# Optimization experiments

Measured on AMD Instinct MI355X. Metric: run time of the kernel, lower is better.

## Reference

```python
import jax, jax.numpy as jnp
import numpy as np

SIGMA = 0.3


def quat_mul(q, r):
    w1, x1, y1, z1 = q[..., 0], q[..., 1], q[..., 2], q[..., 3]
    w2, x2, y2, z2 = r[..., 0], r[..., 1], r[..., 2], r[..., 3]
    return jnp.stack([
        w1 * w2 - x1 * x2 - y1 * y2 - z1 * z2,
        w1 * x2 + x1 * w2 + y1 * z2 - z1 * y2,
        w1 * y2 - x1 * z2 + y1 * w2 + z1 * x2,
        w1 * z2 + x1 * y2 - y1 * x2 + z1 * w2,
    ], axis=-1)


def quat_conjugate(q):
    return q * jnp.array([1.0, -1.0, -1.0, -1.0], dtype=q.dtype)


def quat_rotate(q, v):
    v_quat = jnp.concatenate([jnp.zeros_like(v[..., :1]), v], axis=-1)
    return quat_mul(quat_mul(q, v_quat), quat_conjugate(q))[..., 1:]


def compute_adjacency_batch(x, sigma):
    pos = x[..., :3]
    diff = pos[:, :, None, :] - pos[:, None, :, :]
    dist_sq = jnp.sum(diff * diff, axis=-1)
    A = jnp.exp(-dist_sq / (sigma * sigma))
    I = jnp.eye(A.shape[-1], dtype=A.dtype)[None]
    A = A * (1.0 - I) + I
    return A / jnp.sum(A, axis=-1, keepdims=True)


def _mlp(x, params):
    # params: list of (W, b); GELU (exact erf, torch default) between layers
    n = len(params)
    for i, (W, b) in enumerate(params):
        x = x @ W + b
        if i < n - 1:
            x = jax.nn.gelu(x, approximate=False)
    return x


def _linear_params(key, din, dout, scale=0.05):
    k1, k2 = jax.random.split(key)
    W = jax.random.normal(k1, (din, dout), dtype=jnp.float32) * scale
    b = jax.random.normal(k2, (dout,), dtype=jnp.float32) * scale
    return W, b


def setup_inputs() -> dict:
    key = jax.random.key(0)
    B, N_p, M, D_o, D_p, H = 4, 32768, 64, 13, 13, 256
    ks = jax.random.split(key, 16)
    t = jax.random.uniform(ks[0], (), dtype=jnp.float32)
    x_p = jax.random.normal(ks[1], (B, N_p, D_p), dtype=jnp.float32)
    x_o = jax.random.normal(ks[2], (B, M, D_o), dtype=jnp.float32)
    S = jax.nn.softmax(jax.random.normal(ks[3], (B, N_p, M), dtype=jnp.float32), axis=-1)
    # edge_net: (2*D_o+3+1+1) -> H -> H -> D_o
    ew0, eb0 = _linear_params(ks[4], 2 * D_o + 5, H)
    ew1, eb1 = _linear_params(ks[5], H, H)
    ew2, eb2 = _linear_params(ks[6], H, D_o)
    # f_vel: (2*D_o+1) -> H -> H -> H -> 3
    vw0, vb0 = _linear_params(ks[7], 2 * D_o + 1, H)
    vw1, vb1 = _linear_params(ks[8], H, H)
    vw2, vb2 = _linear_params(ks[9], H, H)
    vw3, vb3 = _linear_params(ks[10], H, 3)
    # f_omega: same sizes
    ow0, ob0 = _linear_params(ks[11], 2 * D_o + 1, H)
    ow1, ob1 = _linear_params(ks[12], H, H)
    ow2, ob2 = _linear_params(ks[13], H, H)
    ow3, ob3 = _linear_params(ks[14], H, 3)
    return dict(t=t, x_p=x_p, x_o=x_o, S=S,
                ew0=ew0, eb0=eb0, ew1=ew1, eb1=eb1, ew2=ew2, eb2=eb2,
                vw0=vw0, vb0=vb0, vw1=vw1, vb1=vb1, vw2=vw2, vb2=vb2, vw3=vw3, vb3=vb3,
                ow0=ow0, ob0=ob0, ow1=ow1, ob1=ob1, ow2=ow2, ob2=ob2, ow3=ow3, ob3=ob3)


def reference(t, x_p, x_o, S,
              ew0, eb0, ew1, eb1, ew2, eb2,
              vw0, vb0, vw1, vb1, vw2, vb2, vw3, vb3,
              ow0, ob0, ow1, ob1, ow2, ob2, ow3, ob3):
    B, N_p, D_p = x_p.shape
    _, N_o, D_o = x_o.shape
    tt = jnp.reshape(jnp.asarray(t, x_o.dtype), ())

    # ---- object-object messaging ----
    A_obj = compute_adjacency_batch(x_o, sigma=SIGMA)          # [B,No,No]
    pos = x_o[..., :3]
    diff = pos[:, None, :, :] - pos[:, :, None, :]             # diff[b,i,j] = pos_j - pos_i
    distance = jnp.linalg.norm(diff, axis=-1, keepdims=True)
    h_i = jnp.broadcast_to(x_o[:, :, None, :], (B, N_o, N_o, D_o))
    h_j = jnp.broadcast_to(x_o[:, None, :, :], (B, N_o, N_o, D_o))
    t_edge = jnp.broadcast_to(tt, (B, N_o, N_o, 1))
    edge_input = jnp.concatenate([h_i, h_j, diff, distance, t_edge], axis=-1)
    edge_message = _mlp(edge_input, [(ew0, eb0), (ew1, eb1), (ew2, eb2)])  # [B,No,No,Do]
    m_obj = jnp.sum(A_obj[..., None] * edge_message, axis=2)   # [B,No,Do]

    COM_obj = x_o[:, :, :3]
    vel_obj = x_o[:, :, 3:6]
    quat_obj = x_o[:, :, 6:10]
    omega_obj = x_o[:, :, 10:13]

    t0 = jnp.broadcast_to(tt, (B, N_o, 1))
    node_in = jnp.concatenate([x_o, m_obj, t0], axis=-1)
    dx_o_vel = _mlp(node_in, [(vw0, vb0), (vw1, vb1), (vw2, vb2), (vw3, vb3)])
    dx_o_omega = _mlp(node_in, [(ow0, ob0), (ow1, ob1), (ow2, ob2), (ow3, ob3)])
    omega_quat = jnp.concatenate([jnp.zeros_like(omega_obj[..., :1]), omega_obj], axis=-1)
    dx_o_quat = 0.5 * quat_mul(omega_quat, quat_obj)
    dx_o = jnp.concatenate([vel_obj, dx_o_vel, dx_o_quat, dx_o_omega], axis=-1)

    # ---- particle rigid-transform branch ----
    pos_t0 = x_p[..., 10:13]
    local = pos_t0[:, :, None, :] - COM_obj[:, None, :, :]     # [B,Np,M,3]
    rot_local = quat_rotate(quat_obj[:, None, :, :], local)    # broadcast quats over particles
    pred_vel = vel_obj[:, None, :, :] + jnp.cross(
        jnp.broadcast_to(omega_obj[:, None, :, :], rot_local.shape), rot_local)
    final_vel = jnp.sum(S[..., None] * pred_vel, axis=2)       # [B,Np,3]

    current_vel = x_p[..., 3:6]
    dpos = final_vel
    dvel = final_vel - current_vel
    dquat = jnp.zeros_like(x_p[..., 6:10])
    dpos_t0 = jnp.zeros_like(x_p[..., 10:13])
    dx_p = jnp.concatenate([dpos, dvel, dquat, dpos_t0], axis=-1)
    return dx_p, dx_o
```

## Files before the change

kernel.cpp:

```cpp
#include <hip/hip_runtime.h>
#include <math.h>

typedef unsigned short u16;
typedef unsigned int   u32;

typedef __attribute__((ext_vector_type(8))) short short8;
typedef __attribute__((ext_vector_type(4))) float f32x4;

static constexpr int CB  = 4;
static constexpr int CNP = 32768;
static constexpr int CM  = 64;
static constexpr int CDO = 13;
static constexpr int CH  = 256;
static constexpr int DXP_ELEMS = CB * CNP * CDO;

static constexpr int WSB_W0 = 16384;
static constexpr int WSB_W1 = 32768;

__device__ __forceinline__ float bf2f(u16 v) { return __uint_as_float(((u32)v) << 16); }
__device__ __forceinline__ u16 f2bf(float f) {
    u32 u = __float_as_uint(f);
    u += 0x7fffu + ((u >> 16) & 1u);
    return (u16)(u >> 16);
}
__device__ __forceinline__ float gelu_f(float x) {
    float y = 0.7978845608028654f * (x + 0.044715f * x * x * x);
    float e = __expf(2.0f * y);
    float t = 1.0f - 2.0f / (e + 1.0f);
    return 0.5f * x * (1.0f + t);
}

__global__ __launch_bounds__(256) void k0_prep(const float* __restrict__ ew0,
                                               const float* __restrict__ ew1,
                                               u16* __restrict__ w0frag,
                                               u16* __restrict__ w1frag) {
    int idx = blockIdx.x * 256 + threadIdx.x;
    if (idx < 8192) {
        int j = idx & 7, lane = (idx >> 3) & 63, nt = idx >> 9;
        int k = (lane >> 4) * 8 + j, n = nt * 16 + (lane & 15);
        float v = (k < 31) ? ew0[k * CH + n] : 0.0f;
        w0frag[idx] = f2bf(v);
    } else if (idx < 73728) {
        int rel = idx - 8192;
        int j = rel & 7, lane = (rel >> 3) & 63, ktnt = rel >> 9;
        int nt = ktnt & 15, kt = ktnt >> 4;
        int k = kt * 32 + (lane >> 4) * 8 + j, n = nt * 16 + (lane & 15);
        w1frag[rel] = f2bf(ew1[k * CH + n]);
    }
}

__global__ __launch_bounds__(256) void k1_edge(const float* __restrict__ xo,
                                               const float* __restrict__ tp,
                                               const float* __restrict__ eb0,
                                               const float* __restrict__ eb1,
                                               const float* __restrict__ ew2,
                                               const float* __restrict__ eb2,
                                               const u16* __restrict__ w0frag,
                                               const u16* __restrict__ w1frag,
                                               float* __restrict__ mobj) {
    __shared__ float sXo[832];
    __shared__ float sAnorm[64];
    __shared__ float sInv;
    __shared__ float sBias[512];
    __shared__ float sW2[3456];
    __shared__ float sMsg[512];
    __shared__ __align__(16) u16 sIn[32 * 40];
    __shared__ __align__(16) u16 sH1[32 * 264];
    __shared__ __align__(16) u16 sH2T[256 * 36];

    const int tid  = threadIdx.x;
    const int blk  = blockIdx.x;
    const int b    = blk >> 6;
    const int i    = blk & 63;
    const int wave = tid >> 6;
    const int lane = tid & 63;
    const int quad = lane >> 4;
    const int mr   = lane & 15;
    const int mtile = wave & 1;
    const int nhalf = wave >> 1;

    for (int idx = tid; idx < 832; idx += 256) sXo[idx] = xo[(size_t)b * 832 + idx];
    sBias[tid]       = eb0[tid];
    sBias[256 + tid] = eb1[tid];
    for (int idx = tid; idx < 3456; idx += 256) sW2[idx] = (idx < 3328) ? ew2[idx] : 0.0f;
    __syncthreads();

    const float pix = sXo[i * 13 + 0], piy = sXo[i * 13 + 1], piz = sXo[i * 13 + 2];
    if (tid < 64) {
        float dx = pix - sXo[tid * 13 + 0];
        float dy = piy - sXo[tid * 13 + 1];
        float dz = piz - sXo[tid * 13 + 2];
        sAnorm[tid] = expf(-(dx * dx + dy * dy + dz * dz) * 11.111111111111111f);
    }
    __syncthreads();
    if (tid == 0) {
        float s = 0.0f;
        #pragma unroll
        for (int q = 0; q < 64; ++q) s += sAnorm[q];
        sInv = 1.0f / s;
    }
    __syncthreads();
    if (tid < 64) sAnorm[tid] *= sInv;
    const float tval = tp[0];

    float msum = (tid < 13) ? eb2[tid] : 0.0f;

    for (int pass = 0; pass < 2; ++pass) {
        const int j0 = pass * 32;
        for (int idx = tid; idx < 1024; idx += 256) {
            int e = idx >> 5, k = idx & 31;
            int j = j0 + e;
            float v;
            if (k < 13) v = sXo[i * 13 + k];
            else if (k < 26) v = sXo[j * 13 + (k - 13)];
            else if (k < 29) { int c = k - 26; v = sXo[j * 13 + c] - sXo[i * 13 + c]; }
            else if (k == 29) {
                float dx = sXo[j * 13 + 0] - pix;
                float dy = sXo[j * 13 + 1] - piy;
                float dz = sXo[j * 13 + 2] - piz;
                v = sqrtf(dx * dx + dy * dy + dz * dz);
            } else if (k == 30) v = tval;
            else v = 0.0f;
            sIn[e * 40 + k] = f2bf(v);
        }
        __syncthreads();

        {
            short8 afrag = *(const short8*)(sIn + (mtile * 16 + mr) * 40 + quad * 8);
            for (int p = 0; p < 4; ++p) {
                int nt = nhalf * 8 + p * 2;
                float bv0 = sBias[nt * 16 + mr];
                float bv1 = sBias[nt * 16 + 16 + mr];
                f32x4 acc0 = { bv0, bv0, bv0, bv0 };
                f32x4 acc1 = { bv1, bv1, bv1, bv1 };
                short8 bf0 = *(const short8*)(w0frag + (nt * 64 + lane) * 8);
                short8 bf1 = *(const short8*)(w0frag + ((nt + 1) * 64 + lane) * 8);
                acc0 = __builtin_amdgcn_mfma_f32_16x16x32_bf16(afrag, bf0, acc0, 0, 0, 0);
                acc1 = __builtin_amdgcn_mfma_f32_16x16x32_bf16(afrag, bf1, acc1, 0, 0, 0);
                #pragma unroll
                for (int r = 0; r < 4; ++r) {
                    int row = mtile * 16 + quad * 4 + r;
                    sH1[row * 264 + nt * 16 + mr]        = f2bf(gelu_f(acc0[r]));
                    sH1[row * 264 + (nt + 1) * 16 + mr]  = f2bf(gelu_f(acc1[r]));
                }
            }
        }
        __syncthreads();

        for (int p = 0; p < 4; ++p) {
            int nt = nhalf * 8 + p * 2;
            float bv0 = sBias[256 + nt * 16 + mr];
            float bv1 = sBias[256 + nt * 16 + 16 + mr];
            f32x4 acc0 = { bv0, bv0, bv0, bv0 };
            f32x4 acc1 = { bv1, bv1, bv1, bv1 };
            #pragma unroll
            for (int kt = 0; kt < 8; ++kt) {
                short8 a  = *(const short8*)(sH1 + (mtile * 16 + mr) * 264 + kt * 32 + quad * 8);
                short8 b0 = *(const short8*)(w1frag + ((kt * 16 + nt) * 64 + lane) * 8);
                short8 b1 = *(const short8*)(w1frag + ((kt * 16 + nt + 1) * 64 + lane) * 8);
                acc0 = __builtin_amdgcn_mfma_f32_16x16x32_bf16(a, b0, acc0, 0, 0, 0);
                acc1 = __builtin_amdgcn_mfma_f32_16x16x32_bf16(a, b1, acc1, 0, 0, 0);
            }
            u16 pk0[4], pk1[4];
            #pragma unroll
            for (int r = 0; r < 4; ++r) { pk0[r] = f2bf(gelu_f(acc0[r])); pk1[r] = f2bf(gelu_f(acc1[r])); }
            int n0 = nt * 16 + mr, n1 = (nt + 1) * 16 + mr;
            int eb = mtile * 16 + quad * 4;
            *(uint2*)(sH2T + n0 * 36 + eb) = *(const uint2*)pk0;
            *(uint2*)(sH2T + n1 * 36 + eb) = *(const uint2*)pk1;
        }
        __syncthreads();

        {
            const int e = tid & 31;
            const int g = tid >> 5;
            float acc0 = 0.0f, acc1 = 0.0f;
            #pragma unroll 8
            for (int n = 0; n < 256; ++n) {
                float h = bf2f(sH2T[n * 36 + e]);
                acc0 = fmaf(h, sW2[n * 13 + g], acc0);
                acc1 = fmaf(h, sW2[n * 13 + g + 8], acc1);
            }
            float aw = sAnorm[j0 + e];
            sMsg[e * 16 + g] = acc0 * aw;
            if (g < 5) sMsg[e * 16 + g + 8] = acc1 * aw;
        }
        __syncthreads();

        if (tid < 13) {
            float s = 0.0f;
            #pragma unroll
            for (int e = 0; e < 32; ++e) s += sMsg[e * 16 + tid];
            msum += s;
        }
        __syncthreads();
    }

    if (tid < 13) mobj[blk * 16 + tid] = msum;
}

__global__ __launch_bounds__(256) void k2_node(const float* __restrict__ xo,
                                               const float* __restrict__ tp,
                                               const float* __restrict__ mobj,
                                               const float* vw0, const float* vb0,
                                               const float* vw1, const float* vb1,
                                               const float* vw2, const float* vb2,
                                               const float* vw3, const float* vb3,
                                               const float* ow0, const float* ob0,
                                               const float* ow1, const float* ob1,
                                               const float* ow2, const float* ob2,
                                               const float* ow3, const float* ob3,
                                               float* __restrict__ out_dxo) {
    __shared__ float sIn[32];
    __shared__ float sA[256];
    __shared__ float sB[256];
    __shared__ float sPart[192];
    __shared__ float sOut[3];

    const int n   = blockIdx.x >> 1;
    const int ml  = blockIdx.x & 1;
    const int tid = threadIdx.x;

    const float* w0 = ml ? ow0 : vw0;  const float* b0 = ml ? ob0 : vb0;
    const float* w1 = ml ? ow1 : vw1;  const float* b1 = ml ? ob1 : vb1;
    const float* w2 = ml ? ow2 : vw2;  const float* b2 = ml ? ob2 : vb2;
    const float* w3 = ml ? ow3 : vw3;  const float* b3 = ml ? ob3 : vb3;

    const float* xrow = xo + (size_t)n * CDO;
    if (tid < 13)       sIn[tid] = xrow[tid];
    else if (tid < 26)  sIn[tid] = mobj[n * 16 + (tid - 13)];
    else if (tid == 26) sIn[26]  = tp[0];
    __syncthreads();

    float a = b0[tid];
    #pragma unroll
    for (int k = 0; k < 27; ++k) a = fmaf(sIn[k], w0[k * CH + tid], a);
    sA[tid] = gelu_f(a);
    __syncthreads();

    a = b1[tid];
    for (int k8 = 0; k8 < 32; ++k8) {
        float wv[8];
        #pragma unroll
        for (int u = 0; u < 8; ++u) wv[u] = w1[(k8 * 8 + u) * CH + tid];
        #pragma unroll
        for (int u = 0; u < 8; ++u) a = fmaf(sA[k8 * 8 + u], wv[u], a);
    }
    sB[tid] = gelu_f(a);
    __syncthreads();

    a = b2[tid];
    for (int k8 = 0; k8 < 32; ++k8) {
        float wv[8];
        #pragma unroll
        for (int u = 0; u < 8; ++u) wv[u] = w2[(k8 * 8 + u) * CH + tid];
        #pragma unroll
        for (int u = 0; u < 8; ++u) a = fmaf(sB[k8 * 8 + u], wv[u], a);
    }
    sA[tid] = gelu_f(a);
    __syncthreads();

    if (tid < 192) {
        int o = tid % 3, seg = tid / 3;
        float p = 0.0f;
        #pragma unroll
        for (int u = 0; u < 4; ++u) {
            int k = seg * 4 + u;
            p = fmaf(sA[k], w3[k * 3 + o], p);
        }
        sPart[tid] = p;
    }
    __syncthreads();
    if (tid < 3) {
        float s = b3[tid];
        for (int seg = 0; seg < 64; ++seg) s += sPart[seg * 3 + tid];
        sOut[tid] = s;
    }
    __syncthreads();

    if (tid == 0) {
        float* o = out_dxo + (size_t)n * CDO;
        if (ml == 0) {
            o[0] = xrow[3]; o[1] = xrow[4]; o[2] = xrow[5];
            o[3] = sOut[0]; o[4] = sOut[1]; o[5] = sOut[2];
        } else {
            float qw = xrow[6], qx = xrow[7], qy = xrow[8], qz = xrow[9];
            float ox = xrow[10], oy = xrow[11], oz = xrow[12];
            o[6] = -0.5f * (ox * qx + oy * qy + oz * qz);
            o[7] =  0.5f * (ox * qw + oy * qz - oz * qy);
            o[8] =  0.5f * (-ox * qz + oy * qw + oz * qx);
            o[9] =  0.5f * (ox * qy - oy * qx + oz * qw);
            o[10] = sOut[0]; o[11] = sOut[1]; o[12] = sOut[2];
        }
    }
}

__global__ __launch_bounds__(256) void k3_part(const float* __restrict__ xp,
                                               const float* __restrict__ S,
                                               const float* __restrict__ xo,
                                               float* __restrict__ out) {
    __shared__ float sXo[832];
    __shared__ float sPar[768];
    __shared__ __align__(16) float sXp[3328];
    __shared__ __align__(16) float sOutF[3328];

    const int tid  = threadIdx.x;
    const int blk  = blockIdx.x;
    const int pid0 = blk << 8;
    const int b    = pid0 >> 15;

    for (int idx = tid; idx < 832; idx += 256) sXo[idx] = xo[(size_t)b * 832 + idx];
    {
        const float4* src = (const float4*)(xp) + (size_t)blk * 832;
        float4* dst = (float4*)sXp;
        for (int idx = tid; idx < 832; idx += 256) dst[idx] = src[idx];
    }
    __syncthreads();

    if (tid < 64) {
        const int r = tid * CDO;
        float cx = sXo[r + 0], cy = sXo[r + 1], cz = sXo[r + 2];
        float vx = sXo[r + 3], vy = sXo[r + 4], vz = sXo[r + 5];
        float qw = sXo[r + 6], qx = sXo[r + 7], qy = sXo[r + 8], qz = sXo[r + 9];
        float ox = sXo[r + 10], oy = sXo[r + 11], oz = sXo[r + 12];
        float s2 = qw * qw - (qx * qx + qy * qy + qz * qz);
        float R00 = s2 + 2.f*qx*qx,        R01 = 2.f*qx*qy - 2.f*qw*qz, R02 = 2.f*qx*qz + 2.f*qw*qy;
        float R10 = 2.f*qy*qx + 2.f*qw*qz, R11 = s2 + 2.f*qy*qy,        R12 = 2.f*qy*qz - 2.f*qw*qx;
        float R20 = 2.f*qz*qx - 2.f*qw*qy, R21 = 2.f*qz*qy + 2.f*qw*qx, R22 = s2 + 2.f*qz*qz;
        float W00 = -oz*R10 + oy*R20, W01 = -oz*R11 + oy*R21, W02 = -oz*R12 + oy*R22;
        float W10 =  oz*R00 - ox*R20, W11 =  oz*R01 - ox*R21, W12 =  oz*R02 - ox*R22;
        float W20 = -oy*R00 + ox*R10, W21 = -oy*R01 + ox*R11, W22 = -oy*R02 + ox*R12;
        float* par = sPar + tid * 12;
        par[0] = vx - (W00*cx + W01*cy + W02*cz);
        par[1] = vy - (W10*cx + W11*cy + W12*cz);
        par[2] = vz - (W20*cx + W21*cy + W22*cz);
        par[3] = W00; par[4]  = W01; par[5]  = W02;
        par[6] = W10; par[7]  = W11; par[8]  = W12;
        par[9] = W20; par[10] = W21; par[11] = W22;
    }
    __syncthreads();

    const int p13 = tid * CDO;
    const float cvx = sXp[p13 + 3],  cvy = sXp[p13 + 4],  cvz = sXp[p13 + 5];
    const float px  = sXp[p13 + 10], py  = sXp[p13 + 11], pz  = sXp[p13 + 12];

    float fvx = 0.0f, fvy = 0.0f, fvz = 0.0f;
    const size_t pid = (size_t)pid0 + tid;
    const float4* srow = (const float4*)(S) + pid * 16;
    #pragma unroll
    for (int g = 0; g < 16; ++g) {
        float4 sv = srow[g];
        float sf[4] = { sv.x, sv.y, sv.z, sv.w };
        #pragma unroll
        for (int h = 0; h < 4; ++h) {
            float s = sf[h];
            const float* pp = sPar + (g * 4 + h) * 12;
            float tx = pp[0] + pp[3] * px + pp[4]  * py + pp[5]  * pz;
            float ty = pp[1] + pp[6] * px + pp[7]  * py + pp[8]  * pz;
            float tz = pp[2] + pp[9] * px + pp[10] * py + pp[11] * pz;
            fvx = fmaf(s, tx, fvx);
            fvy = fmaf(s, ty, fvy);
            fvz = fmaf(s, tz, fvz);
        }
    }

    sOutF[p13 + 0] = fvx;
    sOutF[p13 + 1] = fvy;
    sOutF[p13 + 2] = fvz;
    sOutF[p13 + 3] = fvx - cvx;
    sOutF[p13 + 4] = fvy - cvy;
    sOutF[p13 + 5] = fvz - cvz;
    #pragma unroll
    for (int q = 6; q < 13; ++q) sOutF[p13 + q] = 0.0f;
    __syncthreads();
    {
        float4* dstg = (float4*)(out) + (size_t)blk * 832;
        const float4* srcl = (const float4*)sOutF;
        for (int idx = tid; idx < 832; idx += 256) dstg[idx] = srcl[idx];
    }
}

extern "C" void kernel_launch(void* const* d_in, const int* in_sizes, int n_in,
                              void* d_out, int out_size, void* d_ws, size_t ws_size,
                              hipStream_t stream) {
    const float* t  = (const float*)d_in[0];
    const float* xp = (const float*)d_in[1];
    const float* xo = (const float*)d_in[2];
    const float* S  = (const float*)d_in[3];
    float* mobj  = (float*)d_ws;
    u16* w0frag  = (u16*)((char*)d_ws + WSB_W0);
    u16* w1frag  = (u16*)((char*)d_ws + WSB_W1);
    float* out = (float*)d_out;

    hipLaunchKernelGGL(k0_prep, dim3(288), dim3(256), 0, stream,
                       (const float*)d_in[4], (const float*)d_in[6], w0frag, w1frag);
    hipLaunchKernelGGL(k1_edge, dim3(256), dim3(256), 0, stream,
                       xo, t,
                       (const float*)d_in[5], (const float*)d_in[7],
                       (const float*)d_in[8], (const float*)d_in[9],
                       w0frag, w1frag, mobj);
    hipLaunchKernelGGL(k2_node, dim3(512), dim3(256), 0, stream,
                       xo, t, mobj,
                       (const float*)d_in[10], (const float*)d_in[11],
                       (const float*)d_in[12], (const float*)d_in[13],
                       (const float*)d_in[14], (const float*)d_in[15],
                       (const float*)d_in[16], (const float*)d_in[17],
                       (const float*)d_in[18], (const float*)d_in[19],
                       (const float*)d_in[20], (const float*)d_in[21],
                       (const float*)d_in[22], (const float*)d_in[23],
                       (const float*)d_in[24], (const float*)d_in[25],
                       out + DXP_ELEMS);
    hipLaunchKernelGGL(k3_part, dim3(512), dim3(256), 0, stream,
                       xp, S, xo, out);
}
```

Before: 205.9 us.

## Batch node MLPs onto bf16 MFMA and use MFMA for edge output layer

```diff
diff --git a/kernel.cpp b/kernel.cpp
--- a/kernel.cpp
+++ b/kernel.cpp
@@ -14,8 +14,19 @@
 static constexpr int CH  = 256;
 static constexpr int DXP_ELEMS = CB * CNP * CDO;
 
-static constexpr int WSB_W0 = 16384;
-static constexpr int WSB_W1 = 32768;
+static constexpr int WSB_FRAG = 16384;
+static constexpr int F_EW0 = 0;
+static constexpr int F_EW1 = 8192;
+static constexpr int F_EW2 = 73728;
+static constexpr int F_VW0 = 77824;
+static constexpr int F_VW1 = 86016;
+static constexpr int F_VW2 = 151552;
+static constexpr int F_VW3 = 217088;
+static constexpr int F_OW0 = 221184;
+static constexpr int F_OW1 = 229376;
+static constexpr int F_OW2 = 294912;
+static constexpr int F_OW3 = 360448;
+static constexpr int F_TOTAL = 364544;
 
 __device__ __forceinline__ float bf2f(u16 v) { return __uint_as_float(((u32)v) << 16); }
 __device__ __forceinline__ u16 f2bf(float f) {
@@ -30,43 +41,54 @@
     return 0.5f * x * (1.0f + t);
 }
 
-__global__ __launch_bounds__(256) void k0_prep(const float* __restrict__ ew0,
-                                               const float* __restrict__ ew1,
-                                               u16* __restrict__ w0frag,
-                                               u16* __restrict__ w1frag) {
+struct Segs { const float* src[11]; };
+
+__constant__
+static __device__ const int SEG_BASE[12] = {0, 8192, 73728, 77824, 86016, 151552,
+                                            217088, 221184, 229376, 294912, 360448, 364544};
+static __device__ const int SEG_K[11]  = {31, 256, 256, 27, 256, 256, 256, 27, 256, 256, 256};
+static __device__ const int SEG_N[11]  = {256, 256, 13, 256, 256, 256, 3, 256, 256, 256, 3};
+static __device__ const int SEG_NT[11] = {16, 16, 1, 16, 16, 16, 1, 16, 16, 16, 1};
+
+__global__ __launch_bounds__(256) void k0_prep(Segs segs, float* __restrict__ ws,
+                                               u16* __restrict__ wsFrag) {
     int idx = blockIdx.x * 256 + threadIdx.x;
-    if (idx < 8192) {
-        int j = idx & 7, lane = (idx >> 3) & 63, nt = idx >> 9;
-        int k = (lane >> 4) * 8 + j, n = nt * 16 + (lane & 15);
-        float v = (k < 31) ? ew0[k * CH + n] : 0.0f;
-        w0frag[idx] = f2bf(v);
-    } else if (idx < 73728) {
-        int rel = idx - 8192;
-        int j = rel & 7, lane = (rel >> 3) & 63, ktnt = rel >> 9;
-        int nt = ktnt & 15, kt = ktnt >> 4;
-        int k = kt * 32 + (lane >> 4) * 8 + j, n = nt * 16 + (lane & 15);
-        w1frag[rel] = f2bf(ew1[k * CH + n]);
-    }
+    if (idx < 4096) { ws[idx] = 0.0f; return; }
+    int f = idx - 4096;
+    if (f >= F_TOTAL) return;
+    int s = 0;
+    while (f >= SEG_BASE[s + 1]) ++s;
+    int rel = f - SEG_BASE[s];
+    int j = rel & 7, lane = (rel >> 3) & 63, t = rel >> 9;
+    int NT = SEG_NT[s];
+    int nt = (NT == 16) ? (t & 15) : 0;
+    int kt = (NT == 16) ? (t >> 4) : t;
+    int k = kt * 32 + ((lane >> 4) << 3) + j;
+    int n = nt * 16 + (lane & 15);
+    int K = SEG_K[s], N = SEG_N[s];
+    float v = (k < K && n < N) ? segs.src[s][k * N + n] : 0.0f;
+    wsFrag[f] = f2bf(v);
 }
 
 __global__ __launch_bounds__(256) void k1_edge(const float* __restrict__ xo,
                                                const float* __restrict__ tp,
                                                const float* __restrict__ eb0,
                                                const float* __restrict__ eb1,
-                                               const float* __restrict__ ew2,
                                                const float* __restrict__ eb2,
-                                               const u16* __restrict__ w0frag,
-                                               const u16* __restrict__ w1frag,
+                                               const u16* __restrict__ wsFrag,
                                                float* __restrict__ mobj) {
     __shared__ float sXo[832];
     __shared__ float sAnorm[64];
     __shared__ float sInv;
     __shared__ float sBias[512];
-    __shared__ float sW2[3456];
     __shared__ float sMsg[512];
     __shared__ __align__(16) u16 sIn[32 * 40];
     __shared__ __align__(16) u16 sH1[32 * 264];
-    __shared__ __align__(16) u16 sH2T[256 * 36];
+    __shared__ __align__(16) u16 sH2[32 * 264];
+
+    const u16* w0frag = wsFrag + F_EW0;
+    const u16* w1frag = wsFrag + F_EW1;
+    const u16* w2frag = wsFrag + F_EW2;
 
     const int tid  = threadIdx.x;
     const int blk  = blockIdx.x;
@@ -82,7 +104,6 @@
     for (int idx = tid; idx < 832; idx += 256) sXo[idx] = xo[(size_t)b * 832 + idx];
     sBias[tid]       = eb0[tid];
     sBias[256 + tid] = eb1[tid];
-    for (int idx = tid; idx < 3456; idx += 256) sW2[idx] = (idx < 3328) ? ew2[idx] : 0.0f;
     __syncthreads();
 
     const float pix = sXo[i * 13 + 0], piy = sXo[i * 13 + 1], piz = sXo[i * 13 + 2];
@@ -127,6 +148,7 @@
 
         {
             short8 afrag = *(const short8*)(sIn + (mtile * 16 + mr) * 40 + quad * 8);
+            #pragma unroll
             for (int p = 0; p < 4; ++p) {
                 int nt = nhalf * 8 + p * 2;
                 float bv0 = sBias[nt * 16 + mr];
@@ -140,13 +162,14 @@
                 #pragma unroll
                 for (int r = 0; r < 4; ++r) {
                     int row = mtile * 16 + quad * 4 + r;
-                    sH1[row * 264 + nt * 16 + mr]        = f2bf(gelu_f(acc0[r]));
-                    sH1[row * 264 + (nt + 1) * 16 + mr]  = f2bf(gelu_f(acc1[r]));
+                    sH1[row * 264 + nt * 16 + mr]       = f2bf(gelu_f(acc0[r]));
+                    sH1[row * 264 + (nt + 1) * 16 + mr] = f2bf(gelu_f(acc1[r]));
                 }
             }
         }
         __syncthreads();
 
+        #pragma unroll
         for (int p = 0; p < 4; ++p) {
             int nt = nhalf * 8 + p * 2;
             float bv0 = sBias[256 + nt * 16 + mr];
@@ -161,29 +184,28 @@
                 acc0 = __builtin_amdgcn_mfma_f32_16x16x32_bf16(a, b0, acc0, 0, 0, 0);
                 acc1 = __builtin_amdgcn_mfma_f32_16x16x32_bf16(a, b1, acc1, 0, 0, 0);
             }
-            u16 pk0[4], pk1[4];
-            #pragma unroll
-            for (int r = 0; r < 4; ++r) { pk0[r] = f2bf(gelu_f(acc0[r])); pk1[r] = f2bf(gelu_f(acc1[r])); }
-            int n0 = nt * 16 + mr, n1 = (nt + 1) * 16 + mr;
-            int eb = mtile * 16 + quad * 4;
-            *(uint2*)(sH2T + n0 * 36 + eb) = *(const uint2*)pk0;
-            *(uint2*)(sH2T + n1 * 36 + eb) = *(const uint2*)pk1;
+            #pragma unroll
+            for (int r = 0; r < 4; ++r) {
+                int row = mtile * 16 + quad * 4 + r;
+                sH2[row * 264 + nt * 16 + mr]       = f2bf(gelu_f(acc0[r]));
+                sH2[row * 264 + (nt + 1) * 16 + mr] = f2bf(gelu_f(acc1[r]));
+            }
         }
         __syncthreads();
 
-        {
-            const int e = tid & 31;
-            const int g = tid >> 5;
-            float acc0 = 0.0f, acc1 = 0.0f;
-            #pragma unroll 8
-            for (int n = 0; n < 256; ++n) {
-                float h = bf2f(sH2T[n * 36 + e]);
-                acc0 = fmaf(h, sW2[n * 13 + g], acc0);
-                acc1 = fmaf(h, sW2[n * 13 + g + 8], acc1);
-            }
-            float aw = sAnorm[j0 + e];
-            sMsg[e * 16 + g] = acc0 * aw;
-            if (g < 5) sMsg[e * 16 + g + 8] = acc1 * aw;
+        if (nhalf == 0) {
+            f32x4 acc = { 0.0f, 0.0f, 0.0f, 0.0f };
+            #pragma unroll
+            for (int kt = 0; kt < 8; ++kt) {
+                short8 a = *(const short8*)(sH2 + (mtile * 16 + mr) * 264 + kt * 32 + quad * 8);
+                short8 bf = *(const short8*)(w2frag + (kt * 64 + lane) * 8);
+                acc = __builtin_amdgcn_mfma_f32_16x16x32_bf16(a, bf, acc, 0, 0, 0);
+            }
+            #pragma unroll
+            for (int r = 0; r < 4; ++r) {
+                int e = mtile * 16 + quad * 4 + r;
+                sMsg[e * 16 + mr] = acc[r] * sAnorm[j0 + e];
+            }
         }
         __syncthreads();
 
@@ -202,87 +224,157 @@
 __global__ __launch_bounds__(256) void k2_node(const float* __restrict__ xo,
                                                const float* __restrict__ tp,
                                                const float* __restrict__ mobj,
-                                               const float* vw0, const float* vb0,
-                                               const float* vw1, const float* vb1,
-                                               const float* vw2, const float* vb2,
-                                               const float* vw3, const float* vb3,
-                                               const float* ow0, const float* ob0,
-                                               const float* ow1, const float* ob1,
-                                               const float* ow2, const float* ob2,
-                                               const float* ow3, const float* ob3,
+                                               const float* __restrict__ vb0,
+                                               const float* __restrict__ vb1,
+                                               const float* __restrict__ vb2,
+                                               const float* __restrict__ vb3,
+                                               const float* __restrict__ ob0,
+                                               const float* __restrict__ ob1,
+                                               const float* __restrict__ ob2,
+                                               const float* __restrict__ ob3,
+                                               const u16* __restrict__ wsFrag,
                                                float* __restrict__ out_dxo) {
-    __shared__ float sIn[32];
-    __shared__ float sA[256];
-    __shared__ float sB[256];
-    __shared__ float sPart[192];
-    __shared__ float sOut[3];
-
-    const int n   = blockIdx.x >> 1;
-    const int ml  = blockIdx.x & 1;
-    const int tid = threadIdx.x;
-
-    const float* w0 = ml ? ow0 : vw0;  const float* b0 = ml ? ob0 : vb0;
-    const float* w1 = ml ? ow1 : vw1;  const float* b1 = ml ? ob1 : vb1;
-    const float* w2 = ml ? ow2 : vw2;  const float* b2 = ml ? ob2 : vb2;
-    const float* w3 = ml ? ow3 : vw3;  const float* b3 = ml ? ob3 : vb3;
-
-    const float* xrow = xo + (size_t)n * CDO;
-    if (tid < 13)       sIn[tid] = xrow[tid];
-    else if (tid < 26)  sIn[tid] = mobj[n * 16 + (tid - 13)];
-    else if (tid == 26) sIn[26]  = tp[0];
-    __syncthreads();
-
-    float a = b0[tid];
+    __shared__ __align__(16) u16 sIn[64 * 40];
+    __shared__ __align__(16) u16 sHa[64 * 264];
+    __shared__ __align__(16) u16 sHb[64 * 264];
+    __shared__ float sBias[772];
+    __shared__ float sOut3[256];
+
+    const int tid  = threadIdx.x;
+    const int bid  = blockIdx.x;
+    const int ml   = bid >> 2;
+    const int m0   = (bid & 3) * 64;
+    const int wave = tid >> 6;
+    const int lane = tid & 63;
+    const int quad = lane >> 4;
+    const int mr   = lane & 15;
+
+    const u16* w0f = wsFrag + (ml ? F_OW0 : F_VW0);
+    const u16* w1f = wsFrag + (ml ? F_OW1 : F_VW1);
+    const u16* w2f = wsFrag + (ml ? F_OW2 : F_VW2);
+    const u16* w3f = wsFrag + (ml ? F_OW3 : F_VW3);
+    const float* b0 = ml ? ob0 : vb0;
+    const float* b1 = ml ? ob1 : vb1;
+    const float* b2 = ml ? ob2 : vb2;
+    const float* b3 = ml ? ob3 : vb3;
+
+    sBias[tid]       = b0[tid];
+    sBias[256 + tid] = b1[tid];
+    sBias[512 + tid] = b2[tid];
+    if (tid < 3) sBias[768 + tid] = b3[tid];
+
+    const float tval = tp[0];
+    for (int idx = tid; idx < 64 * 32; idx += 256) {
+        int m = idx >> 5, k = idx & 31;
+        int n = m0 + m;
+        float v;
+        if (k < 13)      v = xo[n * 13 + k];
+        else if (k < 26) v = mobj[n * 16 + (k - 13)];
+        else if (k == 26) v = tval;
+        else v = 0.0f;
+        sIn[m * 40 + k] = f2bf(v);
+    }
+    __syncthreads();
+
+    {
+        short8 afrag = *(const short8*)(sIn + (wave * 16 + mr) * 40 + quad * 8);
+        #pragma unroll
+        for (int p = 0; p < 8; ++p) {
+            int nt = p * 2;
+            float bv0 = sBias[nt * 16 + mr];
+            float bv1 = sBias[nt * 16 + 16 + mr];
+            f32x4 acc0 = { bv0, bv0, bv0, bv0 };
+            f32x4 acc1 = { bv1, bv1, bv1, bv1 };
+            short8 bf0 = *(const short8*)(w0f + (nt * 64 + lane) * 8);
+            short8 bf1 = *(const short8*)(w0f + ((nt + 1) * 64 + lane) * 8);
+            acc0 = __builtin_amdgcn_mfma_f32_16x16x32_bf16(afrag, bf0, acc0, 0, 0, 0);
+            acc1 = __builtin_amdgcn_mfma_f32_16x16x32_bf16(afrag, bf1, acc1, 0, 0, 0);
+            #pragma unroll
+            for (int r = 0; r < 4; ++r) {
+                int row = wave * 16 + quad * 4 + r;
+                sHa[row * 264 + nt * 16 + mr]       = f2bf(gelu_f(acc0[r]));
+                sHa[row * 264 + (nt + 1) * 16 + mr] = f2bf(gelu_f(acc1[r]));
+            }
+        }
+    }
+    __syncthreads();
+
     #pragma unroll
-    for (int k = 0; k < 27; ++k) a = fmaf(sIn[k], w0[k * CH + tid], a);
-    sA[tid] = gelu_f(a);
-    __syncthreads();
-
-    a = b1[tid];
-    for (int k8 = 0; k8 < 32; ++k8) {
-        float wv[8];
-        #pragma unroll
-        for (int u = 0; u < 8; ++u) wv[u] = w1[(k8 * 8 + u) * CH + tid];
-        #pragma unroll
-        for (int u = 0; u < 8; ++u) a = fmaf(sA[k8 * 8 + u], wv[u], a);
-    }
-    sB[tid] = gelu_f(a);
-    __syncthreads();
-
-    a = b2[tid];
-    for (int k8 = 0; k8 < 32; ++k8) {
-        float wv[8];
-        #pragma unroll
-        for (int u = 0; u < 8; ++u) wv[u] = w2[(k8 * 8 + u) * CH + tid];
-        #pragma unroll
-        for (int u = 0; u < 8; ++u) a = fmaf(sB[k8 * 8 + u], wv[u], a);
-    }
-    sA[tid] = gelu_f(a);
-    __syncthreads();
-
-    if (tid < 192) {
-        int o = tid % 3, seg = tid / 3;
-        float p = 0.0f;
-        #pragma unroll
-        for (int u = 0; u < 4; ++u) {
-            int k = seg * 4 + u;
-            p = fmaf(sA[k], w3[k * 3 + o], p);
-        }
-        sPart[tid] = p;
-    }
-    __syncthreads();
-    if (tid < 3) {
-        float s = b3[tid];
-        for (int seg = 0; seg < 64; ++seg) s += sPart[seg * 3 + tid];
-        sOut[tid] = s;
-    }
-    __syncthreads();
-
-    if (tid == 0) {
+    for (int p = 0; p < 8; ++p) {
+        int nt = p * 2;
+        float bv0 = sBias[256 + nt * 16 + mr];
+        float bv1 = sBias[256 + nt * 16 + 16 + mr];
+        f32x4 acc0 = { bv0, bv0, bv0, bv0 };
+        f32x4 acc1 = { bv1, bv1, bv1, bv1 };
+        #pragma unroll
+        for (int kt = 0; kt < 8; ++kt) {
+            short8 a  = *(const short8*)(sHa + (wave * 16 + mr) * 264 + kt * 32 + quad * 8);
+            short8 bf0 = *(const short8*)(w1f + ((kt * 16 + nt) * 64 + lane) * 8);
+            short8 bf1 = *(const short8*)(w1f + ((kt * 16 + nt + 1) * 64 + lane) * 8);
+            acc0 = __builtin_amdgcn_mfma_f32_16x16x32_bf16(a, bf0, acc0, 0, 0, 0);
+            acc1 = __builtin_amdgcn_mfma_f32_16x16x32_bf16(a, bf1, acc1, 0, 0, 0);
+        }
+        #pragma unroll
+        for (int r = 0; r < 4; ++r) {
+            int row = wave * 16 + quad * 4 + r;
+            sHb[row * 264 + nt * 16 + mr]       = f2bf(gelu_f(acc0[r]));
+            sHb[row * 264 + (nt + 1) * 16 + mr] = f2bf(gelu_f(acc1[r]));
+        }
+    }
+    __syncthreads();
+
+    #pragma unroll
+    for (int p = 0; p < 8; ++p) {
+        int nt = p * 2;
+        float bv0 = sBias[512 + nt * 16 + mr];
+        float bv1 = sBias[512 + nt * 16 + 16 + mr];
+        f32x4 acc0 = { bv0, bv0, bv0, bv0 };
+        f32x4 acc1 = { bv1, bv1, bv1, bv1 };
+        #pragma unroll
+        for (int kt = 0; kt < 8; ++kt) {
+            short8 a  = *(const short8*)(sHb + (wave * 16 + mr) * 264 + kt * 32 + quad * 8);
+            short8 bf0 = *(const short8*)(w2f + ((kt * 16 + nt) * 64 + lane) * 8);
+            short8 bf1 = *(const short8*)(w2f + ((kt * 16 + nt + 1) * 64 + lane) * 8);
+            acc0 = __builtin_amdgcn_mfma_f32_16x16x32_bf16(a, bf0, acc0, 0, 0, 0);
+            acc1 = __builtin_amdgcn_mfma_f32_16x16x32_bf16(a, bf1, acc1, 0, 0, 0);
+        }
+        #pragma unroll
+        for (int r = 0; r < 4; ++r) {
+            int row = wave * 16 + quad * 4 + r;
+            sHa[row * 264 + nt * 16 + mr]       = f2bf(gelu_f(acc0[r]));
+            sHa[row * 264 + (nt + 1) * 16 + mr] = f2bf(gelu_f(acc1[r]));
+        }
+    }
+    __syncthreads();
+
+    {
+        float bv = (mr < 3) ? sBias[768 + mr] : 0.0f;
+        f32x4 acc = { bv, bv, bv, bv };
+        #pragma unroll
+        for (int kt = 0; kt < 8; ++kt) {
+            short8 a  = *(const short8*)(sHa + (wave * 16 + mr) * 264 + kt * 32 + quad * 8);
+            short8 bf = *(const short8*)(w3f + (kt * 64 + lane) * 8);
+            acc = __builtin_amdgcn_mfma_f32_16x16x32_bf16(a, bf, acc, 0, 0, 0);
+        }
+        if (mr < 3) {
+            #pragma unroll
+            for (int r = 0; r < 4; ++r) {
+                int row = wave * 16 + quad * 4 + r;
+                sOut3[row * 4 + mr] = acc[r];
+            }
+        }
+    }
+    __syncthreads();
+
+    if (tid < 64) {
+        int n = m0 + tid;
+        const float* xrow = xo + (size_t)n * CDO;
         float* o = out_dxo + (size_t)n * CDO;
         if (ml == 0) {
             o[0] = xrow[3]; o[1] = xrow[4]; o[2] = xrow[5];
-            o[3] = sOut[0]; o[4] = sOut[1]; o[5] = sOut[2];
+            o[3] = sOut3[tid * 4 + 0];
+            o[4] = sOut3[tid * 4 + 1];
+            o[5] = sOut3[tid * 4 + 2];
         } else {
             float qw = xrow[6], qx = xrow[7], qy = xrow[8], qz = xrow[9];
             float ox = xrow[10], oy = xrow[11], oz = xrow[12];
@@ -290,7 +382,9 @@
             o[7] =  0.5f * (ox * qw + oy * qz - oz * qy);
             o[8] =  0.5f * (-ox * qz + oy * qw + oz * qx);
             o[9] =  0.5f * (ox * qy - oy * qx + oz * qw);
-            o[10] = sOut[0]; o[11] = sOut[1]; o[12] = sOut[2];
+            o[10] = sOut3[tid * 4 + 0];
+            o[11] = sOut3[tid * 4 + 1];
+            o[12] = sOut3[tid * 4 + 2];
         }
     }
 }
@@ -387,29 +481,35 @@
     const float* xp = (const float*)d_in[1];
     const float* xo = (const float*)d_in[2];
     const float* S  = (const float*)d_in[3];
-    float* mobj  = (float*)d_ws;
-    u16* w0frag  = (u16*)((char*)d_ws + WSB_W0);
-    u16* w1frag  = (u16*)((char*)d_ws + WSB_W1);
+    float* mobj = (float*)d_ws;
+    u16* wsFrag = (u16*)((char*)d_ws + WSB_FRAG);
     float* out = (float*)d_out;
 
-    hipLaunchKernelGGL(k0_prep, dim3(288), dim3(256), 0, stream,
-                       (const float*)d_in[4], (const float*)d_in[6], w0frag, w1frag);
+    Segs segs;
+    segs.src[0]  = (const float*)d_in[4];
+    segs.src[1]  = (const float*)d_in[6];
+    segs.src[2]  = (const float*)d_in[8];
+    segs.src[3]  = (const float*)d_in[10];
+    segs.src[4]  = (const float*)d_in[12];
+    segs.src[5]  = (const float*)d_in[14];
+    segs.src[6]  = (const float*)d_in[16];
+    segs.src[7]  = (const float*)d_in[18];
+    segs.src[8]  = (const float*)d_in[20];
+    segs.src[9]  = (const float*)d_in[22];
+    segs.src[10] = (const float*)d_in[24];
+
+    hipLaunchKernelGGL(k0_prep, dim3(1440), dim3(256), 0, stream, segs, mobj, wsFrag);
     hipLaunchKernelGGL(k1_edge, dim3(256), dim3(256), 0, stream,
                        xo, t,
-                       (const float*)d_in[5], (const float*)d_in[7],
-                       (const float*)d_in[8], (const float*)d_in[9],
-                       w0frag, w1frag, mobj);
-    hipLaunchKernelGGL(k2_node, dim3(512), dim3(256), 0, stream,
+                       (const float*)d_in[5], (const float*)d_in[7], (const float*)d_in[9],
+                       wsFrag, mobj);
+    hipLaunchKernelGGL(k2_node, dim3(8), dim3(256), 0, stream,
                        xo, t, mobj,
-                       (const float*)d_in[10], (const float*)d_in[11],
-                       (const float*)d_in[12], (const float*)d_in[13],
-                       (const float*)d_in[14], (const float*)d_in[15],
-                       (const float*)d_in[16], (const float*)d_in[17],
-                       (const float*)d_in[18], (const float*)d_in[19],
-                       (const float*)d_in[20], (const float*)d_in[21],
-                       (const float*)d_in[22], (const float*)d_in[23],
-                       (const float*)d_in[24], (const float*)d_in[25],
-                       out + DXP_ELEMS);
+                       (const float*)d_in[11], (const float*)d_in[13],
+                       (const float*)d_in[15], (const float*)d_in[17],
+                       (const float*)d_in[19], (const float*)d_in[21],
+                       (const float*)d_in[23], (const float*)d_in[25],
+                       wsFrag, out + DXP_ELEMS);
     hipLaunchKernelGGL(k3_part, dim3(512), dim3(256), 0, stream,
                        xp, S, xo, out);
 }
```

Result: faster. 191.1 us (-7.2%).
